# Optimization experiments

Hardware: AMD Instinct MI355X
Metric: run time of the kernel (lower is better)

Reference implementation:

```python
import jax, jax.numpy as jnp
import numpy as np

BN_EPS = 1e-5

def _conv(x, w, pad):
    return jax.lax.conv_general_dilated(
        x, w, window_strides=(1, 1), padding=[(pad, pad), (pad, pad)],
        dimension_numbers=('NCHW', 'OIHW', 'NCHW'))

def setup_inputs() -> dict:
    key = jax.random.key(0)
    ks = jax.random.split(key, 6)
    B, C1, C2, H, W, k = 4, 128, 256, 64, 64, 3
    N = k * k
    x = jax.random.normal(ks[0], (B, C1, H, W), jnp.float32)
    pw_w = jax.random.normal(ks[1], (C2, C1, 1, 1), jnp.float32) * 0.05
    bn_gamma = jnp.ones((C2,), jnp.float32)
    bn_beta = jnp.zeros((C2,), jnp.float32)
    bn_mean = jax.random.normal(ks[2], (C2,), jnp.float32) * 0.1
    bn_var = jax.random.uniform(ks[3], (C2,), jnp.float32, minval=0.5, maxval=1.5)
    off_w = jax.random.normal(ks[4], (2 * N, C2, 3, 3), jnp.float32) * 0.01
    off_b = jnp.zeros((2 * N,), jnp.float32)
    dcn_w = jax.random.normal(ks[5], (C2, C2, k, k), jnp.float32) * 0.02
    return dict(x=x, pw_w=pw_w, bn_gamma=bn_gamma, bn_beta=bn_beta,
                bn_mean=bn_mean, bn_var=bn_var, off_w=off_w, off_b=off_b,
                dcn_w=dcn_w)

def reference(x, pw_w, bn_gamma, bn_beta, bn_mean, bn_var, off_w, off_b, dcn_w):
    B, C1, H, W = x.shape
    C2 = pw_w.shape[0]
    k = dcn_w.shape[-1]
    N = k * k
    # ---- 1x1 pointwise conv + BatchNorm (eval mode), act=False ----
    xp = _conv(x, pw_w, 0)
    scale = bn_gamma * jax.lax.rsqrt(bn_var + BN_EPS)
    xp = xp * scale[None, :, None, None] + (bn_beta - bn_mean * scale)[None, :, None, None]
    # ---- offset prediction conv: [B, 2N, H, W]; first N = dy, last N = dx ----
    offset = _conv(xp, off_w, 1) + off_b[None, :, None, None]
    off_y, off_x = offset[:, :N], offset[:, N:]
    # ---- sampling positions p = p0 + p_n + offset ----
    gy, gx = jnp.meshgrid(jnp.arange(H, dtype=jnp.float32),
                          jnp.arange(W, dtype=jnp.float32), indexing='ij')
    kk = jnp.arange(k, dtype=jnp.float32) - (k // 2)
    ky, kx = jnp.meshgrid(kk, kk, indexing='ij')
    py = gy[None, None] + ky.reshape(N)[None, :, None, None] + off_y  # [B,N,H,W]
    px = gx[None, None] + kx.reshape(N)[None, :, None, None] + off_x
    py = jnp.clip(py, 0.0, H - 1.0)
    px = jnp.clip(px, 0.0, W - 1.0)

    def sample_one(img, py_b, px_b):  # img [C2,H,W], py/px [N,H,W]
        y0 = jnp.floor(py_b)
        x0 = jnp.floor(px_b)
        wy = py_b - y0
        wx = px_b - x0
        y0i = y0.astype(jnp.int32)
        x0i = x0.astype(jnp.int32)
        y1i = jnp.minimum(y0i + 1, H - 1)
        x1i = jnp.minimum(x0i + 1, W - 1)
        flat = img.reshape(C2, H * W)
        def g(yy, xx):
            idx = (yy * W + xx).reshape(-1)
            return flat[:, idx].reshape(C2, N, H, W)
        v00 = g(y0i, x0i); v01 = g(y0i, x1i)
        v10 = g(y1i, x0i); v11 = g(y1i, x1i)
        wy = wy[None]; wx = wx[None]
        return (v00 * (1 - wy) * (1 - wx) + v01 * (1 - wy) * wx +
                v10 * wy * (1 - wx) + v11 * wy * wx)

    sampled = jax.vmap(sample_one)(xp, py, px)  # [B,C2,N,H,W]
    # ---- deformable conv = weighted sum over kernel points ----
    out = jnp.einsum('bcnhw,ocn->bohw', sampled, dcn_w.reshape(C2, C2, N))
    return jax.nn.silu(out)
```

## Files before the change

kernel.cpp:

```cpp
#include <hip/hip_runtime.h>
#include <math.h>

#define XP_F   0
#define OFF_F  4194304
#define XPH_F  4489216
#define WTB_F  6586368

typedef short bf16x8 __attribute__((ext_vector_type(8)));
typedef float f32x4 __attribute__((ext_vector_type(4)));

__device__ inline unsigned short f2b(float f) {
    union { float f; unsigned u; } v; v.f = f;
    unsigned r = v.u + 0x7FFF + ((v.u >> 16) & 1);
    return (unsigned short)(r >> 16);
}
__device__ inline float b2f(unsigned short h) {
    union { unsigned u; float f; } v; v.u = ((unsigned)h) << 16; return v.f;
}

__global__ __launch_bounds__(256) void k0_prep(const float* __restrict__ dcn,
                                               const float* __restrict__ offb,
                                               unsigned short* __restrict__ wTb,
                                               float* __restrict__ off) {
    int idx = blockIdx.x * 256 + threadIdx.x;
    int n = idx >> 16, o = (idx >> 8) & 255, c = idx & 255;
    wTb[idx] = f2b(dcn[(o * 256 + c) * 9 + n]);
    if (idx < 294912) {
        int j = (idx >> 12) % 18;
        off[idx] = offb[j];
    }
}

__global__ __launch_bounds__(256, 4) void k1_pw_bn(const float* __restrict__ x,
                                                   const float* __restrict__ pw,
                                                   const float* __restrict__ gamma,
                                                   const float* __restrict__ beta,
                                                   const float* __restrict__ mean,
                                                   const float* __restrict__ var,
                                                   float* __restrict__ xp,
                                                   unsigned short* __restrict__ xph) {
    __shared__ float wl[128 * 64];
    int t = threadIdx.x;
    int m0 = blockIdx.x * 64;
    int b = m0 >> 12;
    int hw = (m0 & 4095) + (t & 63);
    int q = t >> 6;
    int c2base = blockIdx.y * 64;

    for (int i = 0; i < 32; ++i) {
        int idx = t + 256 * i;
        int c2l = idx >> 7, kk = idx & 127;
        wl[kk * 64 + c2l] = pw[(c2base + c2l) * 128 + kk];
    }
    __syncthreads();

    float acc[16];
#pragma unroll
    for (int i = 0; i < 16; ++i) acc[i] = 0.f;

    const float* xb = x + (b * 128) * 4096 + hw;
    for (int kk = 0; kk < 128; kk += 8) {
        float xv[8];
#pragma unroll
        for (int u = 0; u < 8; ++u) xv[u] = xb[(kk + u) * 4096];
#pragma unroll
        for (int u = 0; u < 8; ++u) {
            const float4* w4 = (const float4*)&wl[(kk + u) * 64 + q * 16];
#pragma unroll
            for (int i = 0; i < 4; ++i) {
                float4 wv = w4[i];
                acc[i * 4 + 0] += xv[u] * wv.x;
                acc[i * 4 + 1] += xv[u] * wv.y;
                acc[i * 4 + 2] += xv[u] * wv.z;
                acc[i * 4 + 3] += xv[u] * wv.w;
            }
        }
    }
    bf16x8 r0, r1;
#pragma unroll
    for (int i = 0; i < 16; ++i) {
        int c2 = c2base + q * 16 + i;
        float s = gamma[c2] * rsqrtf(var[c2] + 1e-5f);
        float v = acc[i] * s + (beta[c2] - mean[c2] * s);
        xp[((b * 256 + c2) << 12) + hw] = v;
        if (i < 8) r0[i] = (short)f2b(v); else r1[i - 8] = (short)f2b(v);
    }
    unsigned short* hb = xph + (((b << 12) + hw) << 8) + c2base + q * 16;
    *(bf16x8*)hb = r0;
    *(bf16x8*)(hb + 8) = r1;
}

__global__ __launch_bounds__(256) void k2_off(const float* __restrict__ xp,
                                              const float* __restrict__ offw,
                                              float* __restrict__ off) {
    __shared__ float xl[3 * 32 * 66];
    __shared__ float wl[9 * 18 * 32];
    int t = threadIdx.x;
    int bx = blockIdx.x;
    int b = bx >> 9, h = (bx >> 3) & 63, cs = bx & 7;
    int w = t & 63, jset = t >> 6;
    const int jbase_a[4] = {0, 5, 10, 14};
    const int jcnt_a[4] = {5, 5, 4, 4};
    int jbase = jbase_a[jset], jcnt = jcnt_a[jset];
    float acc[5] = {0.f, 0.f, 0.f, 0.f, 0.f};
    int cbase = cs * 32;

    for (int idx = t; idx < 3 * 32 * 66; idx += 256) {
        int dy = idx / 2112, rem = idx % 2112;
        int c = rem / 66, col = rem % 66;
        int y = h + dy - 1, wc = col - 1;
        float v = 0.f;
        if ((unsigned)y < 64u && (unsigned)wc < 64u)
            v = xp[((b * 256 + cbase + c) << 12) + y * 64 + wc];
        xl[idx] = v;
    }
    for (int idx = t; idx < 18 * 32 * 9; idx += 256) {
        int j = idx / 288, c = (idx / 9) % 32, tap = idx % 9;
        wl[(tap * 18 + j) * 32 + c] = offw[(j * 256 + cbase + c) * 9 + tap];
    }
    __syncthreads();
#pragma unroll
    for (int tap = 0; tap < 9; ++tap) {
        int dy = tap / 3, dx = tap % 3;
        const float* xrow = &xl[dy * 2112 + (w + dx)];
        const float4* wrow = (const float4*)&wl[(tap * 18 + jbase) * 32];
#pragma unroll
        for (int c4 = 0; c4 < 8; ++c4) {
            float xv0 = xrow[(c4 * 4 + 0) * 66];
            float xv1 = xrow[(c4 * 4 + 1) * 66];
            float xv2 = xrow[(c4 * 4 + 2) * 66];
            float xv3 = xrow[(c4 * 4 + 3) * 66];
#pragma unroll
            for (int jj = 0; jj < 5; ++jj) {
                if (jj < jcnt) {
                    float4 wv = wrow[jj * 8 + c4];
                    acc[jj] += xv0 * wv.x + xv1 * wv.y + xv2 * wv.z + xv3 * wv.w;
                }
            }
        }
    }
    for (int jj = 0; jj < 5; ++jj) {
        if (jj < jcnt)
            atomicAdd(&off[((b * 18 + jbase + jj) << 12) + h * 64 + w], acc[jj]);
    }
}

__global__ __launch_bounds__(512, 4) void k3_dcn(const unsigned short* __restrict__ xph,
                                                 const float* __restrict__ off,
                                                 const unsigned short* __restrict__ wTb,
                                                 float* __restrict__ out) {
    __shared__ int   i00[288], i01[288], i10[288], i11[288];
    __shared__ float w00[288], w01[288], w10[288], w11[288];
    __shared__ unsigned short smp[2][16 * 64 * 8];

    int t = threadIdx.x;
    int orig = blockIdx.x;
    int bx = (orig & 7) * 64 + (orig >> 3);
    int b = bx >> 7, h = (bx >> 1) & 63, wh = (bx & 1) * 32;
    int wv = t >> 6, l = t & 63;
    const unsigned short* xb = xph + (b << 20);

    if (t < 288) {
        int n = t >> 5, p = t & 31;
        int w = wh + p;
        float oy = off[((b * 18 + n) << 12) + h * 64 + w];
        float ox = off[((b * 18 + n + 9) << 12) + h * 64 + w];
        float py = (float)(h + n / 3 - 1) + oy;
        float px = (float)(w + n % 3 - 1) + ox;
        py = fminf(fmaxf(py, 0.f), 63.f);
        px = fminf(fmaxf(px, 0.f), 63.f);
        float fy = floorf(py), fx = floorf(px);
        int y0 = (int)fy, x0 = (int)fx;
        float wy = py - fy, wx = px - fx;
        int y1 = min(y0 + 1, 63), x1 = min(x0 + 1, 63);
        i00[t] = (y0 * 64 + x0) << 8;  i01[t] = (y0 * 64 + x1) << 8;
        i10[t] = (y1 * 64 + x0) << 8;  i11[t] = (y1 * 64 + x1) << 8;
        w00[t] = (1.f - wy) * (1.f - wx);  w01[t] = (1.f - wy) * wx;
        w10[t] = wy * (1.f - wx);          w11[t] = wy * wx;
    }
    __syncthreads();

    bf16x8 g[2][4];

    auto stage_issue = [&](int tap) {
#pragma unroll
        for (int ku = 0; ku < 2; ++ku) {
            int unit = t + ku * 512;
            int px = unit >> 5, cg = unit & 31;
            int sb = tap * 32 + px;
            int c = cg << 3;
            g[ku][0] = *(const bf16x8*)(xb + i00[sb] + c);
            g[ku][1] = *(const bf16x8*)(xb + i01[sb] + c);
            g[ku][2] = *(const bf16x8*)(xb + i10[sb] + c);
            g[ku][3] = *(const bf16x8*)(xb + i11[sb] + c);
        }
    };
    auto stage_write = [&](int tap) {
        int bu = tap & 1;
#pragma unroll
        for (int ku = 0; ku < 2; ++ku) {
            int unit = t + ku * 512;
            int px = unit >> 5, cg = unit & 31;
            int sb = tap * 32 + px;
            float b00 = w00[sb], b01 = w01[sb], b10 = w10[sb], b11 = w11[sb];
            bf16x8 r;
#pragma unroll
            for (int j = 0; j < 8; ++j) {
                float v = b00 * b2f((unsigned short)g[ku][0][j]) +
                          b01 * b2f((unsigned short)g[ku][1][j]) +
                          b10 * b2f((unsigned short)g[ku][2][j]) +
                          b11 * b2f((unsigned short)g[ku][3][j]);
                r[j] = (short)f2b(v);
            }
            int F = (px >> 4) * 8 + (cg >> 2);
            int lane = (cg & 3) * 16 + (px & 15);
            *(bf16x8*)&smp[bu][(F * 64 + (lane ^ (F & 7))) << 3] = r;
        }
    };

    stage_issue(0);
    stage_write(0);
    __syncthreads();

    f32x4 acc[2][2];
#pragma unroll
    for (int i = 0; i < 2; ++i)
#pragma unroll
        for (int j = 0; j < 2; ++j) acc[i][j] = (f32x4)0.f;

    int arow = l & 15, areg = l >> 4;
    for (int tap = 0; tap < 9; ++tap) {
        if (tap < 8) stage_issue(tap + 1);
        int bu = tap & 1;
        const unsigned short* wbase =
            wTb + (tap * 256 + wv * 32 + arow) * 256 + areg * 8;
        __builtin_amdgcn_s_setprio(1);
#pragma unroll
        for (int ks = 0; ks < 8; ++ks) {
            bf16x8 a0 = *(const bf16x8*)(wbase + ks * 32);
            bf16x8 a1 = *(const bf16x8*)(wbase + 16 * 256 + ks * 32);
#pragma unroll
            for (int pt = 0; pt < 2; ++pt) {
                int F = pt * 8 + ks;
                bf16x8 bfr = *(const bf16x8*)
                    &smp[bu][(F * 64 + (l ^ (F & 7))) << 3];
                acc[0][pt] = __builtin_amdgcn_mfma_f32_16x16x32_bf16(a0, bfr, acc[0][pt], 0, 0, 0);
                acc[1][pt] = __builtin_amdgcn_mfma_f32_16x16x32_bf16(a1, bfr, acc[1][pt], 0, 0, 0);
            }
        }
        __builtin_amdgcn_s_setprio(0);
        if (tap < 8) stage_write(tap + 1);
        __syncthreads();
    }

#pragma unroll
    for (int ot = 0; ot < 2; ++ot)
#pragma unroll
        for (int pt = 0; pt < 2; ++pt) {
            int px = wh + pt * 16 + (l & 15);
#pragma unroll
            for (int j = 0; j < 4; ++j) {
                int o = wv * 32 + ot * 16 + (l >> 4) * 4 + j;
                float a = acc[ot][pt][j];
                out[((b * 256 + o) << 12) + h * 64 + px] = a / (1.f + expf(-a));
            }
        }
}

extern "C" void kernel_launch(void* const* d_in, const int* in_sizes, int n_in,
                              void* d_out, int out_size, void* d_ws, size_t ws_size,
                              hipStream_t stream) {
    const float* x     = (const float*)d_in[0];
    const float* pw    = (const float*)d_in[1];
    const float* gamma = (const float*)d_in[2];
    const float* beta  = (const float*)d_in[3];
    const float* mean  = (const float*)d_in[4];
    const float* var   = (const float*)d_in[5];
    const float* offw  = (const float*)d_in[6];
    const float* offb  = (const float*)d_in[7];
    const float* dcn   = (const float*)d_in[8];
    float* ws = (float*)d_ws;
    float* xp  = ws + XP_F;
    float* off = ws + OFF_F;
    unsigned short* xph = (unsigned short*)(ws + XPH_F);
    unsigned short* wTb = (unsigned short*)(ws + WTB_F);
    float* out = (float*)d_out;

    hipLaunchKernelGGL(k0_prep, dim3(2304), dim3(256), 0, stream, dcn, offb, wTb, off);
    hipLaunchKernelGGL(k1_pw_bn, dim3(256, 4), dim3(256), 0, stream,
                       x, pw, gamma, beta, mean, var, xp, xph);
    hipLaunchKernelGGL(k2_off, dim3(2048), dim3(256), 0, stream, xp, offw, off);
    hipLaunchKernelGGL(k3_dcn, dim3(512), dim3(512), 0, stream, xph, off, wTb, out);
}
```

Before: 258.2 us.

## Replace offset atomics with partial-sum reduction and remap DCN gather work

The offset conv kernel now writes per-channel-slice partial sums to a workspace buffer, and a new reduction kernel adds them together with the bias, replacing the global float atomics and the bias pre-initialisation. The DCN kernel remaps each thread to a fixed pixel and channel groups that match the MFMA B-fragment layout, so each thread reads one set of bilinear indices and weights per tap. Sched barriers are added around the gather and blend phases. The pointwise-conv weight staging is also changed to coalesced shared-memory writes. The cost is an extra kernel launch and a larger workspace for the partial buffer.

After: 285.2 us. +10.4%, slower.

```diff
diff --git a/kernel.cpp b/kernel.cpp
--- a/kernel.cpp
+++ b/kernel.cpp
@@ -5,6 +5,7 @@
 #define OFF_F  4194304
 #define XPH_F  4489216
 #define WTB_F  6586368
+#define PART_F 6881280
 
 typedef short bf16x8 __attribute__((ext_vector_type(8)));
 typedef float f32x4 __attribute__((ext_vector_type(4)));
@@ -19,16 +20,10 @@
 }
 
 __global__ __launch_bounds__(256) void k0_prep(const float* __restrict__ dcn,
-                                               const float* __restrict__ offb,
-                                               unsigned short* __restrict__ wTb,
-                                               float* __restrict__ off) {
+                                               unsigned short* __restrict__ wTb) {
     int idx = blockIdx.x * 256 + threadIdx.x;
     int n = idx >> 16, o = (idx >> 8) & 255, c = idx & 255;
     wTb[idx] = f2b(dcn[(o * 256 + c) * 9 + n]);
-    if (idx < 294912) {
-        int j = (idx >> 12) % 18;
-        off[idx] = offb[j];
-    }
 }
 
 __global__ __launch_bounds__(256, 4) void k1_pw_bn(const float* __restrict__ x,
@@ -49,8 +44,8 @@
 
     for (int i = 0; i < 32; ++i) {
         int idx = t + 256 * i;
-        int c2l = idx >> 7, kk = idx & 127;
-        wl[kk * 64 + c2l] = pw[(c2base + c2l) * 128 + kk];
+        int kk = idx >> 6, c2l = idx & 63;
+        wl[idx] = pw[(c2base + c2l) * 128 + kk];
     }
     __syncthreads();
 
@@ -90,9 +85,9 @@
     *(bf16x8*)(hb + 8) = r1;
 }
 
-__global__ __launch_bounds__(256) void k2_off(const float* __restrict__ xp,
-                                              const float* __restrict__ offw,
-                                              float* __restrict__ off) {
+__global__ __launch_bounds__(256) void k2a_off(const float* __restrict__ xp,
+                                               const float* __restrict__ offw,
+                                               float* __restrict__ part) {
     __shared__ float xl[3 * 32 * 66];
     __shared__ float wl[9 * 18 * 32];
     int t = threadIdx.x;
@@ -141,8 +136,19 @@
     }
     for (int jj = 0; jj < 5; ++jj) {
         if (jj < jcnt)
-            atomicAdd(&off[((b * 18 + jbase + jj) << 12) + h * 64 + w], acc[jj]);
-    }
+            part[(((cs * 4 + b) * 18 + jbase + jj) << 12) + h * 64 + w] = acc[jj];
+    }
+}
+
+__global__ __launch_bounds__(256) void k2b_red(const float* __restrict__ part,
+                                               const float* __restrict__ offb,
+                                               float* __restrict__ off) {
+    int i = blockIdx.x * 256 + threadIdx.x;
+    int j = (i >> 12) % 18;
+    float s = offb[j];
+#pragma unroll
+    for (int cs = 0; cs < 8; ++cs) s += part[cs * 294912 + i];
+    off[i] = s;
 }
 
 __global__ __launch_bounds__(512, 4) void k3_dcn(const unsigned short* __restrict__ xph,
@@ -180,29 +186,32 @@
     }
     __syncthreads();
 
+    int pt_p = wv & 1;
+    int ks0 = wv >> 1;
+    int px_p = pt_p * 16 + (l & 15);
+    int cgl = l >> 4;
+
     bf16x8 g[2][4];
 
     auto stage_issue = [&](int tap) {
+        int sb = tap * 32 + px_p;
+        int a00 = i00[sb], a01 = i01[sb], a10 = i10[sb], a11 = i11[sb];
 #pragma unroll
         for (int ku = 0; ku < 2; ++ku) {
-            int unit = t + ku * 512;
-            int px = unit >> 5, cg = unit & 31;
-            int sb = tap * 32 + px;
-            int c = cg << 3;
-            g[ku][0] = *(const bf16x8*)(xb + i00[sb] + c);
-            g[ku][1] = *(const bf16x8*)(xb + i01[sb] + c);
-            g[ku][2] = *(const bf16x8*)(xb + i10[sb] + c);
-            g[ku][3] = *(const bf16x8*)(xb + i11[sb] + c);
+            int ks = ks0 + ku * 4;
+            int c = (ks * 4 + cgl) << 3;
+            g[ku][0] = *(const bf16x8*)(xb + a00 + c);
+            g[ku][1] = *(const bf16x8*)(xb + a01 + c);
+            g[ku][2] = *(const bf16x8*)(xb + a10 + c);
+            g[ku][3] = *(const bf16x8*)(xb + a11 + c);
         }
     };
     auto stage_write = [&](int tap) {
         int bu = tap & 1;
+        int sb = tap * 32 + px_p;
+        float b00 = w00[sb], b01 = w01[sb], b10 = w10[sb], b11 = w11[sb];
 #pragma unroll
         for (int ku = 0; ku < 2; ++ku) {
-            int unit = t + ku * 512;
-            int px = unit >> 5, cg = unit & 31;
-            int sb = tap * 32 + px;
-            float b00 = w00[sb], b01 = w01[sb], b10 = w10[sb], b11 = w11[sb];
             bf16x8 r;
 #pragma unroll
             for (int j = 0; j < 8; ++j) {
@@ -212,13 +221,13 @@
                           b11 * b2f((unsigned short)g[ku][3][j]);
                 r[j] = (short)f2b(v);
             }
-            int F = (px >> 4) * 8 + (cg >> 2);
-            int lane = (cg & 3) * 16 + (px & 15);
-            *(bf16x8*)&smp[bu][(F * 64 + (lane ^ (F & 7))) << 3] = r;
+            int F = pt_p * 8 + ks0 + ku * 4;
+            *(bf16x8*)&smp[bu][(F * 64 + (l ^ (F & 7))) << 3] = r;
         }
     };
 
     stage_issue(0);
+    __builtin_amdgcn_sched_barrier(0);
     stage_write(0);
     __syncthreads();
 
@@ -231,6 +240,7 @@
     int arow = l & 15, areg = l >> 4;
     for (int tap = 0; tap < 9; ++tap) {
         if (tap < 8) stage_issue(tap + 1);
+        __builtin_amdgcn_sched_barrier(0);
         int bu = tap & 1;
         const unsigned short* wbase =
             wTb + (tap * 256 + wv * 32 + arow) * 256 + areg * 8;
@@ -249,6 +259,7 @@
             }
         }
         __builtin_amdgcn_s_setprio(0);
+        __builtin_amdgcn_sched_barrier(0);
         if (tap < 8) stage_write(tap + 1);
         __syncthreads();
     }
@@ -280,15 +291,17 @@
     const float* offb  = (const float*)d_in[7];
     const float* dcn   = (const float*)d_in[8];
     float* ws = (float*)d_ws;
-    float* xp  = ws + XP_F;
-    float* off = ws + OFF_F;
+    float* xp   = ws + XP_F;
+    float* off  = ws + OFF_F;
     unsigned short* xph = (unsigned short*)(ws + XPH_F);
     unsigned short* wTb = (unsigned short*)(ws + WTB_F);
+    float* part = ws + PART_F;
     float* out = (float*)d_out;
 
-    hipLaunchKernelGGL(k0_prep, dim3(2304), dim3(256), 0, stream, dcn, offb, wTb, off);
+    hipLaunchKernelGGL(k0_prep, dim3(2304), dim3(256), 0, stream, dcn, wTb);
     hipLaunchKernelGGL(k1_pw_bn, dim3(256, 4), dim3(256), 0, stream,
                        x, pw, gamma, beta, mean, var, xp, xph);
-    hipLaunchKernelGGL(k2_off, dim3(2048), dim3(256), 0, stream, xp, offw, off);
+    hipLaunchKernelGGL(k2a_off, dim3(2048), dim3(256), 0, stream, xp, offw, part);
+    hipLaunchKernelGGL(k2b_red, dim3(1152), dim3(256), 0, stream, part, offb, off);
     hipLaunchKernelGGL(k3_dcn, dim3(512), dim3(512), 0, stream, xph, off, wTb, out);
 }
```
